# Optimization experiments

Measured on AMD Instinct MI355X. Metric: run time of the kernel, lower is better.

The kernel has to match this reference:

```python
import jax, jax.numpy as jnp
import numpy as np

SOFTCAP = 15.0
EPS_RMS = 1e-6
EPS_L2 = 1e-12


def rms_norm(x):
    # F.rms_norm without affine weight
    return x * jax.lax.rsqrt(jnp.mean(x * x, axis=-1, keepdims=True) + EPS_RMS)


def l2_normalize(x):
    # F.normalize(dim=-1): x / max(||x||, eps)
    n = jnp.sqrt(jnp.sum(x * x, axis=-1, keepdims=True))
    return x / jnp.maximum(n, EPS_L2)


def setup_inputs() -> dict:
    key = jax.random.key(0)
    ks = jax.random.split(key, 7)
    B, D, H, KVH, HD = 2, 1024, 16, 4, 64
    chunk_start_idx, chunk_len, n_scratchpad = 2048, 2048, 64
    T = chunk_start_idx + chunk_len + n_scratchpad  # 4160
    s = 0.02
    return {
        "x": jax.random.normal(ks[0], (B, T, D), dtype=jnp.float32),
        "Wq": jax.random.normal(ks[1], (D, D), dtype=jnp.float32) * s,
        "Wk": jax.random.normal(ks[2], (KVH * HD, D), dtype=jnp.float32) * s,
        "Wv": jax.random.normal(ks[3], (KVH * HD, D), dtype=jnp.float32) * s,
        "Wo": jax.random.normal(ks[4], (D, D), dtype=jnp.float32) * s,
        "Wfc": jax.random.normal(ks[5], (4 * D, D), dtype=jnp.float32) * s,
        "Wproj": jax.random.normal(ks[6], (D, 4 * D), dtype=jnp.float32) * s,
        "chunk_start_idx": chunk_start_idx,
        "chunk_len": chunk_len,
        "n_scratchpad": n_scratchpad,
    }


def reference(x, Wq, Wk, Wv, Wo, Wfc, Wproj, chunk_start_idx, chunk_len, n_scratchpad):
    B, T, D = x.shape
    H = 16
    KVH = Wk.shape[0] // (D // H)
    HD = D // H
    update_start = chunk_start_idx
    n_update = T - update_start

    x_norm = rms_norm(x)
    x_upd = x_norm[:, update_start:]

    q = (x_upd @ Wq.T).reshape(B, n_update, H, HD).transpose(0, 2, 1, 3)   # [B,H,Q,hd]
    k = (x_norm @ Wk.T).reshape(B, T, KVH, HD).transpose(0, 2, 1, 3)       # [B,KVH,T,hd]
    v = (x_norm @ Wv.T).reshape(B, T, KVH, HD).transpose(0, 2, 1, 3)

    q = l2_normalize(q)
    k = l2_normalize(k)

    if KVH < H:
        rep = H // KVH
        k = jnp.repeat(k, rep, axis=1)
        v = jnp.repeat(v, rep, axis=1)

    scale = 1.0 / jnp.sqrt(jnp.float32(HD))
    scores = jnp.einsum("bhqd,bhkd->bhqk", q, k) * scale
    q_pos = jnp.arange(update_start, T)[:, None]
    kv_pos = jnp.arange(T)[None, :]
    mask = kv_pos <= q_pos  # [Q,T] causal
    scores = jnp.where(mask[None, None], scores, -jnp.inf)
    probs = jax.nn.softmax(scores, axis=-1)
    attn = jnp.einsum("bhqk,bhkd->bhqd", probs, v)             # [B,H,Q,hd]
    attn = attn.transpose(0, 2, 1, 3).reshape(B, n_update, D)

    attn_out = attn @ Wo.T
    attn_out = SOFTCAP * jnp.tanh(attn_out / SOFTCAP)

    x_new = x[:, update_start:] + attn_out
    h = rms_norm(x_new) @ Wfc.T
    h = jnp.square(jax.nn.relu(h))  # nanochat MLP: relu(x)^2
    x_new = x_new + h @ Wproj.T

    if update_start > 0:
        return jnp.concatenate([x[:, :update_start], x_new], axis=1)
    return x_new
```

## Files before the change

### kernel.cpp

```cpp
#include <hip/hip_runtime.h>
#include <hip/hip_bf16.h>

#define B_   2
#define T_   4160
#define D_   1024
#define H_   16
#define KVH_ 4
#define HD_  64
#define UPD  2048
#define NU   2112
#define MQ   (B_*NU)
#define MT   (B_*T_)

typedef unsigned short u16;
typedef __attribute__((ext_vector_type(8))) short bf16x8;
typedef __attribute__((ext_vector_type(4))) float f32x4;
typedef __attribute__((ext_vector_type(4))) unsigned short u16x4;

__device__ __forceinline__ float bf2f(u16 u){ return __uint_as_float(((unsigned)u)<<16); }
__device__ __forceinline__ u16 f2bf(float f){
  unsigned u = __float_as_uint(f);
  u += 0x7FFF + ((u>>16)&1);
  return (u16)(u>>16);
}

__device__ __forceinline__ void gll16(const void* g, void* l){
  __builtin_amdgcn_global_load_lds((const __attribute__((address_space(1))) char*)g,
                                   (__attribute__((address_space(3))) char*)l, 16, 0, 0);
}

__global__ void cast_bf16(const float* __restrict__ in, u16* __restrict__ o, int n){
  int i = blockIdx.x*blockDim.x + threadIdx.x;
  if (i*4 < n){
    float4 v = ((const float4*)in)[i];
    u16x4 u; u.x=f2bf(v.x); u.y=f2bf(v.y); u.z=f2bf(v.z); u.w=f2bf(v.w);
    ((u16x4*)o)[i] = u;
  }
}

__global__ void rmsnorm_kernel(const float* __restrict__ in, u16* __restrict__ obf,
                               float* __restrict__ copy_out, int withcopy){
  int row = blockIdx.x;
  int t = threadIdx.x;
  const float* xr = in + (size_t)row*D_;
  float4 v = ((const float4*)xr)[t];
  float ss = v.x*v.x + v.y*v.y + v.z*v.z + v.w*v.w;
  #pragma unroll
  for (int o=32;o;o>>=1) ss += __shfl_xor(ss, o);
  __shared__ float red[4];
  if ((t&63)==0) red[t>>6] = ss;
  __syncthreads();
  float tot = red[0]+red[1]+red[2]+red[3];
  float sc = rsqrtf(tot*(1.0f/D_) + 1e-6f);
  u16x4 o4; o4.x=f2bf(v.x*sc); o4.y=f2bf(v.y*sc); o4.z=f2bf(v.z*sc); o4.w=f2bf(v.w*sc);
  ((u16x4*)(obf + (size_t)row*D_))[t] = o4;
  if (withcopy && (row % T_) < UPD)
    ((float4*)(copy_out + (size_t)row*D_))[t] = v;
}

__global__ void l2norm_kernel(u16* __restrict__ buf, int nvec){
  int vid = blockIdx.x*4 + (threadIdx.x>>6);
  int ln = threadIdx.x & 63;
  if (vid >= nvec) return;
  u16* p = buf + (size_t)vid*64 + ln;
  float x = bf2f(*p);
  float ss = x*x;
  #pragma unroll
  for (int o=32;o;o>>=1) ss += __shfl_xor(ss, o);
  float n = sqrtf(ss);
  n = (n < 1e-12f) ? 1e-12f : n;
  *p = f2bf(x / n);
}

template<int EPI, int AMAP>
__global__ __launch_bounds__(256) void gemm_bt(
    const u16* __restrict__ A, const u16* __restrict__ Bw, void* __restrict__ C,
    void* __restrict__ aux, int M, int N, int K)
{
  __shared__ alignas(16) u16 sA[2][4096];
  __shared__ alignas(16) u16 sB[2][4096];
  int m0 = blockIdx.y*128, n0 = blockIdx.x*128;
  int tid = threadIdx.x;
  int wv = tid>>6, ln = tid&63;
  int wr = wv>>1, wc = wv&1;
  int lr = ln&15, lg = ln>>4;

  auto stage = [&](int bu, int kt){
    #pragma unroll
    for (int c=0;c<2;c++){
      int ci = c*256 + tid;
      int row = ci>>2, colb = (ci&3)*16;
      int arow = m0 + row;
      if (AMAP==1) arow = (arow/NU)*T_ + UPD + (arow%NU);
      const u16* src = A + (size_t)arow*K + kt*32 + (colb>>1);
      gll16(src, (char*)sA[bu] + (c*256 + wv*64)*16);
    }
    #pragma unroll
    for (int c=0;c<2;c++){
      int ci = c*256 + tid;
      int row = ci>>2, colb = (ci&3)*16;
      const u16* src = Bw + (size_t)(n0+row)*K + kt*32 + (colb>>1);
      gll16(src, (char*)sB[bu] + (c*256 + wv*64)*16);
    }
  };

  f32x4 acc[4][4] = {};
  int nk = K>>5;
  stage(0,0);
  __syncthreads();
  for (int kt=0; kt<nk; ++kt){
    int bu = kt&1;
    if (kt+1<nk) stage(bu^1, kt+1);
    bf16x8 af[4], bfr[4];
    #pragma unroll
    for (int i=0;i<4;i++){
      af[i]  = *(const bf16x8*)&sA[bu][(wr*64 + i*16 + lr)*32 + lg*8];
      bfr[i] = *(const bf16x8*)&sB[bu][(wc*64 + i*16 + lr)*32 + lg*8];
    }
    #pragma unroll
    for (int i=0;i<4;i++)
      #pragma unroll
      for (int j=0;j<4;j++)
        acc[i][j] = __builtin_amdgcn_mfma_f32_16x16x32_bf16(af[i], bfr[j], acc[i][j], 0,0,0);
    __syncthreads();
  }
  #pragma unroll
  for (int i=0;i<4;i++)
    #pragma unroll
    for (int j=0;j<4;j++){
      int grow0 = m0 + wr*64 + i*16 + lg*4;
      int gcol  = n0 + wc*64 + j*16 + lr;
      if (EPI==5){
        if (gcol < 256){
          #pragma unroll
          for (int r=0;r<4;r++)
            ((u16*)C)[(size_t)(grow0+r)*256 + gcol] = f2bf(acc[i][j][r]);
        } else {
          int bb = grow0 / T_;
          int t  = grow0 - bb*T_;
          int kvh = (gcol>>6)&3, d = gcol&63;
          u16x4 pk;
          #pragma unroll
          for (int r=0;r<4;r++) pk[r] = f2bf(acc[i][j][r]);
          *(u16x4*)((u16*)aux + ((size_t)((bb*KVH_+kvh)*64 + d))*T_ + t) = pk;
        }
      } else {
        #pragma unroll
        for (int r=0;r<4;r++){
          int grow = grow0 + r;
          float cv = acc[i][j][r];
          if (EPI==0){
            ((u16*)C)[(size_t)grow*N + gcol] = f2bf(cv);
          } else if (EPI==1){
            int b = grow/NU, t = grow - b*NU;
            float e = __expf(cv*(2.0f/15.0f));
            float val = 15.f*(e-1.f)/(e+1.f) + ((const float*)aux)[((size_t)(b*T_ + UPD + t))*D_ + gcol];
            ((float*)C)[(size_t)grow*N + gcol] = val;
          } else if (EPI==2){
            float rr = cv>0.f ? cv : 0.f;
            ((u16*)C)[(size_t)grow*N + gcol] = f2bf(rr*rr);
          } else {
            int b = grow/NU, t = grow - b*NU;
            float val = ((const float*)aux)[(size_t)grow*N + gcol] + cv;
            ((float*)C)[((size_t)(b*T_ + UPD + t))*D_ + gcol] = val;
          }
        }
      }
    }
}

__global__ __launch_bounds__(256) void attn_kernel(
    const u16* __restrict__ qb, const u16* __restrict__ kb,
    const u16* __restrict__ vT, u16* __restrict__ ab)
{
  __shared__ alignas(16) u16 sK[2][64*64];
  __shared__ alignas(16) u16 sV[2][64*64];
  __shared__ alignas(16) u16 sP[4][32*64];
  int qi_blk = 65 - blockIdx.x;
  int kh = blockIdx.y, b = blockIdx.z;
  int tid = threadIdx.x, wv = tid>>6, ln = tid&63;
  int lr = ln&15, lg = ln>>4;
  int h = kh*4 + wv;
  int qrow0 = qi_blk*32;
  int qbg = UPD + qrow0;

  bf16x8 qf[2][2];
  #pragma unroll
  for (int qi=0;qi<2;qi++){
    const u16* qp = qb + (size_t)(b*NU + qrow0 + qi*16 + lr)*D_ + h*HD_;
    qf[qi][0] = *(const bf16x8*)(qp + lg*8);
    qf[qi][1] = *(const bf16x8*)(qp + 32 + lg*8);
  }
  bf16x8 ones;
  #pragma unroll
  for (int i=0;i<8;i++) ones[i] = (short)0x3F80;

  f32x4 accO[2][4] = {};
  f32x4 accD[2] = {};

  auto stage = [&](int bu, int kt){
    #pragma unroll
    for (int cc=0; cc<2; ++cc){
      int ci = cc*256 + tid;
      int row = ci>>3, slotb = (ci&7)*16;
      int scolb = slotb ^ ((row&7)<<4);
      gll16(kb + (size_t)(b*T_ + kt*64 + row)*256 + kh*HD_ + (scolb>>1),
            (char*)sK[bu] + (cc*256 + wv*64)*16);
    }
    #pragma unroll
    for (int cc=0; cc<2; ++cc){
      int ci = cc*256 + tid;
      int row = ci>>3, slotb = (ci&7)*16;
      int scolb = slotb ^ ((row&7)<<4);
      gll16(vT + (size_t)((b*KVH_+kh)*64 + row)*T_ + kt*64 + (scolb>>1),
            (char*)sV[bu] + (cc*256 + wv*64)*16);
    }
  };

  int nkt = 33 + (qi_blk>>1);
  stage(0,0);
  __syncthreads();
  for (int kt=0; kt<nkt; ++kt){
    int bu = kt&1;
    if (kt+1 < nkt) stage(bu^1, kt+1);
    f32x4 s[2][4];
    #pragma unroll
    for (int qi=0;qi<2;qi++)
      #pragma unroll
      for (int k2=0;k2<4;k2++) s[qi][k2] = (f32x4){0.f,0.f,0.f,0.f};
    #pragma unroll
    for (int k2=0;k2<4;k2++){
      int row = k2*16 + lr;
      int sw = (row&7)<<4;
      bf16x8 k0 = *(const bf16x8*)((const char*)sK[bu] + row*128 + ((lg*16)^sw));
      bf16x8 k1 = *(const bf16x8*)((const char*)sK[bu] + row*128 + ((64+lg*16)^sw));
      #pragma unroll
      for (int qi=0;qi<2;qi++){
        s[qi][k2] = __builtin_amdgcn_mfma_f32_16x16x32_bf16(qf[qi][0], k0, s[qi][k2], 0,0,0);
        s[qi][k2] = __builtin_amdgcn_mfma_f32_16x16x32_bf16(qf[qi][1], k1, s[qi][k2], 0,0,0);
      }
    }
    int ktb = kt*64;
    #pragma unroll
    for (int qi=0;qi<2;qi++)
      #pragma unroll
      for (int k2=0;k2<4;k2++)
        #pragma unroll
        for (int r=0;r<4;r++){
          int kpos = ktb + k2*16 + lr;
          int q_l = qi*16 + lg*4 + r;
          float p = (kpos <= qbg + q_l) ? __expf(s[qi][k2][r]*0.125f) : 0.0f;
          int byte = q_l*128 + ((k2*32 + lr*2) ^ ((q_l&12)<<3));
          *(u16*)((char*)sP[wv] + byte) = f2bf(p);
        }
    bf16x8 pf[2][2];
    #pragma unroll
    for (int qi=0;qi<2;qi++)
      #pragma unroll
      for (int hf=0;hf<2;hf++){
        int byte = (qi*16+lr)*128 + ((hf*64 + lg*16) ^ ((lr&12)<<3));
        pf[qi][hf] = *(const bf16x8*)((const char*)sP[wv] + byte);
      }
    #pragma unroll
    for (int dt=0; dt<4; ++dt){
      int row = dt*16 + lr;
      int sw = (row&7)<<4;
      bf16x8 v0 = *(const bf16x8*)((const char*)sV[bu] + row*128 + ((lg*16)^sw));
      bf16x8 v1 = *(const bf16x8*)((const char*)sV[bu] + row*128 + ((64+lg*16)^sw));
      #pragma unroll
      for (int qi=0;qi<2;qi++){
        accO[qi][dt] = __builtin_amdgcn_mfma_f32_16x16x32_bf16(pf[qi][0], v0, accO[qi][dt], 0,0,0);
        accO[qi][dt] = __builtin_amdgcn_mfma_f32_16x16x32_bf16(pf[qi][1], v1, accO[qi][dt], 0,0,0);
      }
    }
    #pragma unroll
    for (int qi=0;qi<2;qi++){
      accD[qi] = __builtin_amdgcn_mfma_f32_16x16x32_bf16(pf[qi][0], ones, accD[qi], 0,0,0);
      accD[qi] = __builtin_amdgcn_mfma_f32_16x16x32_bf16(pf[qi][1], ones, accD[qi], 0,0,0);
    }
    __syncthreads();
  }
  #pragma unroll
  for (int qi=0;qi<2;qi++)
    #pragma unroll
    for (int dt=0; dt<4; ++dt)
      #pragma unroll
      for (int r=0;r<4;r++){
        float val = accO[qi][dt][r] / accD[qi][r];
        size_t row = (size_t)(b*NU + qrow0 + qi*16 + lg*4 + r);
        ab[row*D_ + h*HD_ + dt*16 + lr] = f2bf(val);
      }
}

extern "C" void kernel_launch(void* const* d_in, const int* in_sizes, int n_in,
                              void* d_out, int out_size, void* d_ws, size_t ws_size,
                              hipStream_t stream)
{
  const float* x     = (const float*)d_in[0];
  const float* Wq    = (const float*)d_in[1];
  const float* Wk    = (const float*)d_in[2];
  const float* Wv    = (const float*)d_in[3];
  const float* Wo    = (const float*)d_in[4];
  const float* Wfc   = (const float*)d_in[5];
  const float* Wproj = (const float*)d_in[6];
  float* out = (float*)d_out;

  char* ws = (char*)d_ws;
  size_t off = 0;
  auto alloc = [&](size_t bytes)->char*{ char* p = ws + off; off += (bytes + 255) & ~(size_t)255; return p; };
  u16* wqb  = (u16*)alloc((size_t)D_*D_*2);
  u16* wkvb = (u16*)alloc((size_t)512*D_*2);
  u16* wob  = (u16*)alloc((size_t)D_*D_*2);
  u16* wfcb = (u16*)alloc((size_t)4096*D_*2);
  u16* wpb  = (u16*)alloc((size_t)D_*4096*2);
  u16* xn   = (u16*)alloc((size_t)MT*D_*2);
  u16* qB   = (u16*)alloc((size_t)MQ*D_*2);
  u16* kB   = (u16*)alloc((size_t)MT*256*2);
  u16* vTb  = (u16*)alloc((size_t)B_*KVH_*64*T_*2);
  u16* aB   = (u16*)alloc((size_t)MQ*D_*2);
  float* xnew = (float*)alloc((size_t)MQ*D_*4);
  u16* xn2  = (u16*)alloc((size_t)MQ*D_*2);
  u16* hB   = (u16*)alloc((size_t)MQ*4096*2);
  (void)ws_size; (void)in_sizes; (void)n_in; (void)out_size;

  cast_bf16<<<1024, 256, 0, stream>>>(Wq, wqb, D_*D_);
  cast_bf16<<<256,  256, 0, stream>>>(Wk, wkvb, 256*D_);
  cast_bf16<<<256,  256, 0, stream>>>(Wv, wkvb + (size_t)256*D_, 256*D_);
  cast_bf16<<<1024, 256, 0, stream>>>(Wo, wob, D_*D_);
  cast_bf16<<<4096, 256, 0, stream>>>(Wfc, wfcb, 4096*D_);
  cast_bf16<<<4096, 256, 0, stream>>>(Wproj, wpb, D_*4096);

  rmsnorm_kernel<<<MT, 256, 0, stream>>>(x, xn, out, 1);

  gemm_bt<0,1><<<dim3(8,33),  256, 0, stream>>>(xn, wqb, qB, nullptr, MQ, D_,  D_);
  gemm_bt<5,0><<<dim3(4,65),  256, 0, stream>>>(xn, wkvb, kB, vTb, MT, 512, D_);

  l2norm_kernel<<<(MQ*H_)/4, 256, 0, stream>>>(qB, MQ*H_);
  l2norm_kernel<<<(MT*KVH_)/4, 256, 0, stream>>>(kB, MT*KVH_);

  attn_kernel<<<dim3(66,4,2), 256, 0, stream>>>(qB, kB, vTb, aB);

  gemm_bt<1,0><<<dim3(8,33),  256, 0, stream>>>(aB, wob, xnew, (void*)x, MQ, D_, D_);

  rmsnorm_kernel<<<MQ, 256, 0, stream>>>(xnew, xn2, nullptr, 0);
  gemm_bt<2,0><<<dim3(32,33), 256, 0, stream>>>(xn2, wfcb, hB, nullptr, MQ, 4096, D_);
  gemm_bt<3,0><<<dim3(8,33),  256, 0, stream>>>(hB, wpb, out, xnew, MQ, D_, 4096);
}
```

Before: 512.7 us.

## Use narrower GEMM tiles, XCD-aware block swizzle, and transposed attention softmax packing

GEMMs gain a BN template parameter, and the small-N GEMMs (Q, KV, O-proj, down-proj) switch to 128x64 tiles, doubling the block count so more CUs are filled. Block indices for the GEMMs and attention are remapped so consecutive blocks spread across the 8 XCDs, aiming for better L2 locality and load balance. In attention, the QK MFMA operands are swapped so each lane holds four consecutive keys. That lets softmax probabilities be packed into 8-byte LDS stores via exp2, and the causal mask is applied only on the final tile. Risks are lower per-block reuse with the narrower tiles and a possible mismatch between the new P layout and the existing swizzle.

```diff
diff --git a/kernel.cpp b/kernel.cpp
--- a/kernel.cpp
+++ b/kernel.cpp
@@ -13,6 +13,7 @@
 #define MT   (B_*T_)
 
 typedef unsigned short u16;
+typedef unsigned int u32;
 typedef __attribute__((ext_vector_type(8))) short bf16x8;
 typedef __attribute__((ext_vector_type(4))) float f32x4;
 typedef __attribute__((ext_vector_type(4))) unsigned short u16x4;
@@ -72,17 +73,23 @@
   *p = f2bf(x / n);
 }
 
-template<int EPI, int AMAP>
+template<int EPI, int AMAP, int BN>
 __global__ __launch_bounds__(256) void gemm_bt(
     const u16* __restrict__ A, const u16* __restrict__ Bw, void* __restrict__ C,
     void* __restrict__ aux, int M, int N, int K)
 {
+  constexpr int MI = (BN==128) ? 4 : 2;
   __shared__ alignas(16) u16 sA[2][4096];
-  __shared__ alignas(16) u16 sB[2][4096];
-  int m0 = blockIdx.y*128, n0 = blockIdx.x*128;
+  __shared__ alignas(16) u16 sB[2][BN*32];
+  unsigned nwg = gridDim.x*gridDim.y;
+  unsigned flat = blockIdx.y*gridDim.x + blockIdx.x;
+  unsigned nf = (flat&7)*(nwg>>3) + (flat>>3);
+  int m0 = (int)(nf / gridDim.x) * 128;
+  int n0 = (int)(nf % gridDim.x) * BN;
   int tid = threadIdx.x;
   int wv = tid>>6, ln = tid&63;
-  int wr = wv>>1, wc = wv&1;
+  int wr = (BN==128) ? (wv>>1) : wv;
+  int wc = (BN==128) ? (wv&1)  : 0;
   int lr = ln&15, lg = ln>>4;
 
   auto stage = [&](int bu, int kt){
@@ -96,7 +103,7 @@
       gll16(src, (char*)sA[bu] + (c*256 + wv*64)*16);
     }
     #pragma unroll
-    for (int c=0;c<2;c++){
+    for (int c=0;c<BN/64;c++){
       int ci = c*256 + tid;
       int row = ci>>2, colb = (ci&3)*16;
       const u16* src = Bw + (size_t)(n0+row)*K + kt*32 + (colb>>1);
@@ -104,31 +111,32 @@
     }
   };
 
-  f32x4 acc[4][4] = {};
+  f32x4 acc[MI][4] = {};
   int nk = K>>5;
   stage(0,0);
   __syncthreads();
   for (int kt=0; kt<nk; ++kt){
     int bu = kt&1;
     if (kt+1<nk) stage(bu^1, kt+1);
-    bf16x8 af[4], bfr[4];
-    #pragma unroll
-    for (int i=0;i<4;i++){
-      af[i]  = *(const bf16x8*)&sA[bu][(wr*64 + i*16 + lr)*32 + lg*8];
-      bfr[i] = *(const bf16x8*)&sB[bu][(wc*64 + i*16 + lr)*32 + lg*8];
-    }
-    #pragma unroll
-    for (int i=0;i<4;i++)
+    bf16x8 af[MI], bfr[4];
+    #pragma unroll
+    for (int i=0;i<MI;i++)
+      af[i]  = *(const bf16x8*)&sA[bu][(wr*(MI*16) + i*16 + lr)*32 + lg*8];
+    #pragma unroll
+    for (int j=0;j<4;j++)
+      bfr[j] = *(const bf16x8*)&sB[bu][(wc*64 + j*16 + lr)*32 + lg*8];
+    #pragma unroll
+    for (int i=0;i<MI;i++)
       #pragma unroll
       for (int j=0;j<4;j++)
         acc[i][j] = __builtin_amdgcn_mfma_f32_16x16x32_bf16(af[i], bfr[j], acc[i][j], 0,0,0);
     __syncthreads();
   }
   #pragma unroll
-  for (int i=0;i<4;i++)
+  for (int i=0;i<MI;i++)
     #pragma unroll
     for (int j=0;j<4;j++){
-      int grow0 = m0 + wr*64 + i*16 + lg*4;
+      int grow0 = m0 + wr*(MI*16) + i*16 + lg*4;
       int gcol  = n0 + wc*64 + j*16 + lr;
       if (EPI==5){
         if (gcol < 256){
@@ -169,6 +177,31 @@
     }
 }
 
+template<bool DIAG>
+__device__ __forceinline__ void sm_pack(const f32x4 (&s)[2][4], char* spw,
+                                        int lr, int lg, int ktb, int qbg){
+  #pragma unroll
+  for (int qi=0;qi<2;qi++)
+    #pragma unroll
+    for (int k2=0;k2<4;k2++){
+      float p[4];
+      #pragma unroll
+      for (int r=0;r<4;r++){
+        float pv = __builtin_amdgcn_exp2f(s[qi][k2][r]*0.18033688f);
+        if (DIAG){
+          int kpos = ktb + k2*16 + lg*4 + r;
+          int qpos = qbg + qi*16 + lr;
+          if (kpos > qpos) pv = 0.f;
+        }
+        p[r] = pv;
+      }
+      __hip_bfloat162 w0 = __float22bfloat162_rn(float2{p[0],p[1]});
+      __hip_bfloat162 w1 = __float22bfloat162_rn(float2{p[2],p[3]});
+      uint2 wd; wd.x = *(u32*)&w0; wd.y = *(u32*)&w1;
+      *(uint2*)(spw + (qi*16+lr)*128 + ((k2*32 + lg*8) ^ ((lr&7)<<4))) = wd;
+    }
+}
+
 __global__ __launch_bounds__(256) void attn_kernel(
     const u16* __restrict__ qb, const u16* __restrict__ kb,
     const u16* __restrict__ vT, u16* __restrict__ ab)
@@ -176,13 +209,17 @@
   __shared__ alignas(16) u16 sK[2][64*64];
   __shared__ alignas(16) u16 sV[2][64*64];
   __shared__ alignas(16) u16 sP[4][32*64];
-  int qi_blk = 65 - blockIdx.x;
-  int kh = blockIdx.y, b = blockIdx.z;
+  unsigned flat = (blockIdx.z*4u + blockIdx.y)*66u + blockIdx.x;
+  unsigned nf = (flat&7)*66u + (flat>>3);
+  int qi_blk = 65 - (int)(nf % 66u);
+  unsigned khb = nf / 66u;
+  int kh = (int)(khb & 3), b = (int)(khb >> 2);
   int tid = threadIdx.x, wv = tid>>6, ln = tid&63;
   int lr = ln&15, lg = ln>>4;
   int h = kh*4 + wv;
   int qrow0 = qi_blk*32;
   int qbg = UPD + qrow0;
+  char* spw = (char*)&sP[wv][0];
 
   bf16x8 qf[2][2];
   #pragma unroll
@@ -236,31 +273,18 @@
       bf16x8 k1 = *(const bf16x8*)((const char*)sK[bu] + row*128 + ((64+lg*16)^sw));
       #pragma unroll
       for (int qi=0;qi<2;qi++){
-        s[qi][k2] = __builtin_amdgcn_mfma_f32_16x16x32_bf16(qf[qi][0], k0, s[qi][k2], 0,0,0);
-        s[qi][k2] = __builtin_amdgcn_mfma_f32_16x16x32_bf16(qf[qi][1], k1, s[qi][k2], 0,0,0);
-      }
-    }
-    int ktb = kt*64;
+        s[qi][k2] = __builtin_amdgcn_mfma_f32_16x16x32_bf16(k0, qf[qi][0], s[qi][k2], 0,0,0);
+        s[qi][k2] = __builtin_amdgcn_mfma_f32_16x16x32_bf16(k1, qf[qi][1], s[qi][k2], 0,0,0);
+      }
+    }
+    if (kt+1 < nkt) sm_pack<false>(s, spw, lr, lg, kt*64, qbg);
+    else            sm_pack<true >(s, spw, lr, lg, kt*64, qbg);
+    bf16x8 pf[2][2];
     #pragma unroll
     for (int qi=0;qi<2;qi++)
       #pragma unroll
-      for (int k2=0;k2<4;k2++)
-        #pragma unroll
-        for (int r=0;r<4;r++){
-          int kpos = ktb + k2*16 + lr;
-          int q_l = qi*16 + lg*4 + r;
-          float p = (kpos <= qbg + q_l) ? __expf(s[qi][k2][r]*0.125f) : 0.0f;
-          int byte = q_l*128 + ((k2*32 + lr*2) ^ ((q_l&12)<<3));
-          *(u16*)((char*)sP[wv] + byte) = f2bf(p);
-        }
-    bf16x8 pf[2][2];
-    #pragma unroll
-    for (int qi=0;qi<2;qi++)
-      #pragma unroll
-      for (int hf=0;hf<2;hf++){
-        int byte = (qi*16+lr)*128 + ((hf*64 + lg*16) ^ ((lr&12)<<3));
-        pf[qi][hf] = *(const bf16x8*)((const char*)sP[wv] + byte);
-      }
+      for (int hf=0;hf<2;hf++)
+        pf[qi][hf] = *(const bf16x8*)(spw + (qi*16+lr)*128 + ((hf*64 + lg*16) ^ ((lr&7)<<4)));
     #pragma unroll
     for (int dt=0; dt<4; ++dt){
       int row = dt*16 + lr;
@@ -332,17 +356,17 @@
 
   rmsnorm_kernel<<<MT, 256, 0, stream>>>(x, xn, out, 1);
 
-  gemm_bt<0,1><<<dim3(8,33),  256, 0, stream>>>(xn, wqb, qB, nullptr, MQ, D_,  D_);
-  gemm_bt<5,0><<<dim3(4,65),  256, 0, stream>>>(xn, wkvb, kB, vTb, MT, 512, D_);
+  gemm_bt<0,1,64><<<dim3(16,33), 256, 0, stream>>>(xn, wqb, qB, nullptr, MQ, D_,  D_);
+  gemm_bt<5,0,64><<<dim3(8,65),  256, 0, stream>>>(xn, wkvb, kB, vTb, MT, 512, D_);
 
   l2norm_kernel<<<(MQ*H_)/4, 256, 0, stream>>>(qB, MQ*H_);
   l2norm_kernel<<<(MT*KVH_)/4, 256, 0, stream>>>(kB, MT*KVH_);
 
   attn_kernel<<<dim3(66,4,2), 256, 0, stream>>>(qB, kB, vTb, aB);
 
-  gemm_bt<1,0><<<dim3(8,33),  256, 0, stream>>>(aB, wob, xnew, (void*)x, MQ, D_, D_);
+  gemm_bt<1,0,64><<<dim3(16,33), 256, 0, stream>>>(aB, wob, xnew, (void*)x, MQ, D_, D_);
 
   rmsnorm_kernel<<<MQ, 256, 0, stream>>>(xnew, xn2, nullptr, 0);
-  gemm_bt<2,0><<<dim3(32,33), 256, 0, stream>>>(xn2, wfcb, hB, nullptr, MQ, 4096, D_);
-  gemm_bt<3,0><<<dim3(8,33),  256, 0, stream>>>(hB, wpb, out, xnew, MQ, D_, 4096);
-}
+  gemm_bt<2,0,128><<<dim3(32,33), 256, 0, stream>>>(xn2, wfcb, hB, nullptr, MQ, 4096, D_);
+  gemm_bt<3,0,64><<<dim3(16,33), 256, 0, stream>>>(hB, wpb, out, xnew, MQ, D_, 4096);
+}
```

After: 445.2 us. 1.15x faster.
